# Kernel optimization log

Measured on AMD Instinct MI355X. Metric: run time of the kernel, lower is better.

Reference implementation:

```python
import jax, jax.numpy as jnp
import numpy as np


def _w1_1d(u, v):
    """POT-style 1D Wasserstein-1 between empirical dists of u and v (uniform weights).

    u, v: (N,) sample values. Follows ot.wasserstein_1d: sort samples, build
    cumulative weights, merge quantile levels, evaluate both quantile functions
    via searchsorted, and integrate |Q_u - Q_v| dq.
    """
    n = u.shape[0]
    u_s = jnp.sort(u)
    v_s = jnp.sort(v)
    # uniform weights -> identical cumulative weights for both distributions
    cw = jnp.cumsum(jnp.full((n,), 1.0 / n, dtype=u.dtype))
    qs = jnp.sort(jnp.concatenate([cw, cw]))  # (2N,) merged quantile levels
    idx = jnp.clip(jnp.searchsorted(cw, qs), 0, n - 1)  # quantile-function lookup
    uq = u_s[idx]
    vq = v_s[idx]
    delta = jnp.diff(qs, prepend=jnp.zeros((1,), dtype=u.dtype))  # dq segments
    return jnp.sum(delta * jnp.abs(uq - vq))


def setup_inputs() -> dict:
    key = jax.random.key(0)
    k1, k2 = jax.random.split(key)
    B, N = 4096, 4096
    return {
        "spectra_predict": jax.random.uniform(k1, (B, N), dtype=jnp.float32),
        "spectra_true": jax.random.uniform(k2, (B, N), dtype=jnp.float32),
    }


def reference(spectra_predict, spectra_true):
    # Original: wasserstein_1d(pred.T, true.T) batches over columns (= rows of
    # the untransposed [B, N] tensors), then mean over the batch.
    losses = jax.vmap(_w1_1d)(spectra_predict, spectra_true)  # (B,)
    return jnp.mean(losses)
```

## Files before the change

kernel.cpp:

```cpp
#include <hip/hip_runtime.h>


constexpr int N_ELEM  = 4096;
constexpr int V       = 32;
constexpr int THREADS = 256;

__device__ __forceinline__ float ce2(float x, float o, bool keep_min) {
    return ((o < x) != keep_min) ? x : o;
}

template<int S>
__device__ __forceinline__ void reg_merge(float r[V]) {
    #pragma unroll
    for (int k = 0; k < V; ++k) {
        if ((k & (S >> 1)) == 0) {
            const int j = k ^ (S - 1);
            const float a = r[k], b = r[j];
            r[k] = fminf(a, b);
            r[j] = fmaxf(a, b);
        }
    }
    #pragma unroll
    for (int s = S >> 2; s >= 1; s >>= 1) {
        #pragma unroll
        for (int k = 0; k < V; ++k) {
            if ((k & s) == 0) {
                const float a = r[k], b = r[k + s];
                r[k]     = fminf(a, b);
                r[k + s] = fmaxf(a, b);
            }
        }
    }
}

__device__ __forceinline__ void reg_tail_asc(float r[V]) {
    #pragma unroll
    for (int s = 16; s >= 1; s >>= 1) {
        #pragma unroll
        for (int k = 0; k < V; ++k) {
            if ((k & s) == 0) {
                const float a = r[k], b = r[k + s];
                r[k]     = fminf(a, b);
                r[k + s] = fmaxf(a, b);
            }
        }
    }
}

template<int CTRL>
__device__ __forceinline__ float dpp_x(float x) {
    return __int_as_float(__builtin_amdgcn_mov_dpp(__float_as_int(x), CTRL, 0xF, 0xF, true));
}
__device__ __forceinline__ float bperm_x(int pa, float x) {
    return __int_as_float(__builtin_amdgcn_ds_bpermute(pa, __float_as_int(x)));
}

template<int M>
__device__ __forceinline__ void xor_pass(float ru[V], float rv[V], int lane) {
    const bool keep_min = (lane & M) == 0;
    if constexpr (M == 1) {
        #pragma unroll
        for (int k = 0; k < V; ++k) {
            ru[k] = ce2(ru[k], dpp_x<0xB1>(ru[k]), keep_min);
            rv[k] = ce2(rv[k], dpp_x<0xB1>(rv[k]), keep_min);
        }
    } else if constexpr (M == 2) {
        #pragma unroll
        for (int k = 0; k < V; ++k) {
            ru[k] = ce2(ru[k], dpp_x<0x4E>(ru[k]), keep_min);
            rv[k] = ce2(rv[k], dpp_x<0x4E>(rv[k]), keep_min);
        }
    } else {
        const int pa = (lane ^ M) << 2;
        #pragma unroll
        for (int k = 0; k < V; ++k) {
            ru[k] = ce2(ru[k], bperm_x(pa, ru[k]), keep_min);
            rv[k] = ce2(rv[k], bperm_x(pa, rv[k]), keep_min);
        }
    }
}

template<int MMAX>
__device__ __forceinline__ void cross_descend(float ru[V], float rv[V], int lane) {
    if constexpr (MMAX >= 32) xor_pass<32>(ru, rv, lane);
    if constexpr (MMAX >= 16) xor_pass<16>(ru, rv, lane);
    if constexpr (MMAX >= 8)  xor_pass<8>(ru, rv, lane);
    if constexpr (MMAX >= 4)  xor_pass<4>(ru, rv, lane);
    if constexpr (MMAX >= 2)  xor_pass<2>(ru, rv, lane);
    if constexpr (MMAX >= 1)  xor_pass<1>(ru, rv, lane);
    reg_tail_asc(ru);
    reg_tail_asc(rv);
}

template<int X>
__device__ __forceinline__ void mirror_pass(float ru[V], float rv[V], int lane) {
    const bool keep_min = (lane & ((X + 1) >> 1)) == 0;
    if constexpr (X == 1) {
        #pragma unroll
        for (int k = 0; k < V / 2; ++k) {
            const int j = V - 1 - k;
            const float ua = dpp_x<0xB1>(ru[j]);
            const float ub = dpp_x<0xB1>(ru[k]);
            ru[k] = ce2(ru[k], ua, keep_min);
            ru[j] = ce2(ru[j], ub, keep_min);
            const float va = dpp_x<0xB1>(rv[j]);
            const float vb = dpp_x<0xB1>(rv[k]);
            rv[k] = ce2(rv[k], va, keep_min);
            rv[j] = ce2(rv[j], vb, keep_min);
        }
    } else {
        const int pa = (lane ^ X) << 2;
        #pragma unroll
        for (int k = 0; k < V / 2; ++k) {
            const int j = V - 1 - k;
            const float ua = bperm_x(pa, ru[j]);
            const float ub = bperm_x(pa, ru[k]);
            ru[k] = ce2(ru[k], ua, keep_min);
            ru[j] = ce2(ru[j], ub, keep_min);
            const float va = bperm_x(pa, rv[j]);
            const float vb = bperm_x(pa, rv[k]);
            rv[k] = ce2(rv[k], va, keep_min);
            rv[j] = ce2(rv[j], vb, keep_min);
        }
    }
}

template<int S>
__device__ __forceinline__ void stage_m(float ru[V], float rv[V], int lane) {
    mirror_pass<(S >> 5) - 1>(ru, rv, lane);
    cross_descend<(S >> 7)>(ru, rv, lane);
}

__global__ __launch_bounds__(THREADS, 5) void w1_rows_kernel(
    const float* __restrict__ pred,
    const float* __restrict__ tru,
    float* __restrict__ out,
    float scale)
{
    __shared__ float xbuf[128 * 33];
    __shared__ float wsum[THREADS / 64];

    const int tid  = threadIdx.x;
    const int t    = tid & 127;
    const int lane = tid & 63;
    const int row  = blockIdx.x * 2 + (tid >> 7);
    const size_t base = (size_t)row * N_ELEM + (size_t)t * V;

    float ru[V], rv[V];
    {
        const float4* u4 = (const float4*)(pred + base);
        const float4* v4 = (const float4*)(tru  + base);
        #pragma unroll
        for (int c = 0; c < V / 4; ++c) {
            float4 a = u4[c], b = v4[c];
            ru[4*c+0] = a.x; ru[4*c+1] = a.y; ru[4*c+2] = a.z; ru[4*c+3] = a.w;
            rv[4*c+0] = b.x; rv[4*c+1] = b.y; rv[4*c+2] = b.z; rv[4*c+3] = b.w;
        }
    }

    reg_merge<2>(ru);  reg_merge<2>(rv);
    reg_merge<4>(ru);  reg_merge<4>(rv);
    reg_merge<8>(ru);  reg_merge<8>(rv);
    reg_merge<16>(ru); reg_merge<16>(rv);
    reg_merge<32>(ru); reg_merge<32>(rv);

    stage_m<64>(ru, rv, lane);
    stage_m<128>(ru, rv, lane);
    stage_m<256>(ru, rv, lane);
    stage_m<512>(ru, rv, lane);
    stage_m<1024>(ru, rv, lane);
    stage_m<2048>(ru, rv, lane);

    {
        const bool is_upper = (t & 64) != 0;
        const int  slot_row = (tid >> 7) * 64;
        const int  my_base  = (slot_row + lane) * 33;
        const int  pa_base  = (slot_row + (63 - lane)) * 33;

        if (is_upper) {
            #pragma unroll
            for (int k = 0; k < V; ++k) xbuf[my_base + k] = ru[k];
        }
        __syncthreads();
        if (!is_upper) {
            #pragma unroll
            for (int k = 0; k < V; ++k) {
                const int  e = V - 1 - k;
                const float o  = xbuf[pa_base + e];
                const float mx = fmaxf(ru[k], o);
                ru[k] = fminf(ru[k], o);
                xbuf[pa_base + e] = mx;
            }
        }
        __syncthreads();
        if (is_upper) {
            #pragma unroll
            for (int k = 0; k < V; ++k) ru[k] = xbuf[my_base + k];
        }

        if (is_upper) {
            #pragma unroll
            for (int k = 0; k < V; ++k) xbuf[my_base + k] = rv[k];
        }
        __syncthreads();
        if (!is_upper) {
            #pragma unroll
            for (int k = 0; k < V; ++k) {
                const int  e = V - 1 - k;
                const float o  = xbuf[pa_base + e];
                const float mx = fmaxf(rv[k], o);
                rv[k] = fminf(rv[k], o);
                xbuf[pa_base + e] = mx;
            }
        }
        __syncthreads();
        if (is_upper) {
            #pragma unroll
            for (int k = 0; k < V; ++k) rv[k] = xbuf[my_base + k];
        }

        cross_descend<32>(ru, rv, lane);
    }

    float part = 0.f;
    #pragma unroll
    for (int k = 0; k < V; ++k) part += fabsf(ru[k] - rv[k]);

    #pragma unroll
    for (int off = 32; off > 0; off >>= 1)
        part += __shfl_down(part, off, 64);

    const int wid = tid >> 6;
    if (lane == 0) wsum[wid] = part;
    __syncthreads();
    if (tid == 0) {
        float tot = wsum[0] + wsum[1] + wsum[2] + wsum[3];
        atomicAdd(out, tot * scale);
    }
}

extern "C" void kernel_launch(void* const* d_in, const int* in_sizes, int n_in,
                              void* d_out, int out_size, void* d_ws, size_t ws_size,
                              hipStream_t stream)
{
    (void)n_in; (void)out_size; (void)d_ws; (void)ws_size;

    const float* pred = (const float*)d_in[0];
    const float* tru  = (const float*)d_in[1];
    float* out = (float*)d_out;

    const int B = in_sizes[0] / N_ELEM;

    hipMemsetAsync(out, 0, sizeof(float), stream);

    const float scale = 1.0f / ((float)N_ELEM * (float)B);
    w1_rows_kernel<<<B / 2, THREADS, 0, stream>>>(pred, tru, out, scale);
}
```

Measured before the change: 253.4 us.

## Replace compare-exchange with sign-flip fmin and DPP mirror/rotate networks

The cross-lane bitonic passes now flip the float sign bit in the upper lanes, so each compare-exchange becomes a single fminf with a negated partner in place of a compare plus select. The sign masks of consecutive passes are combined into one XOR per element. Several passes that used ds_bpermute (mirrors over 4, 8 and 16 lanes, and xor-8) now use DPP controls (quad reverse, row half-mirror, row mirror, row rotate), which cuts LDS permute traffic. Launch bounds drop from 5 to 4 waves to give the compiler more registers. The risks are the extra XOR instructions, lower occupancy, and the correctness of the DPP control encodings.

```diff
diff --git a/kernel.cpp b/kernel.cpp
--- a/kernel.cpp
+++ b/kernel.cpp
@@ -4,10 +4,6 @@
 constexpr int N_ELEM  = 4096;
 constexpr int V       = 32;
 constexpr int THREADS = 256;
-
-__device__ __forceinline__ float ce2(float x, float o, bool keep_min) {
-    return ((o < x) != keep_min) ? x : o;
-}
 
 template<int S>
 __device__ __forceinline__ void reg_merge(float r[V]) {
@@ -46,6 +42,10 @@
         }
     }
 }
+__device__ __forceinline__ void tail2(float ru[V], float rv[V]) {
+    reg_tail_asc(ru);
+    reg_tail_asc(rv);
+}
 
 template<int CTRL>
 __device__ __forceinline__ float dpp_x(float x) {
@@ -55,83 +55,68 @@
     return __int_as_float(__builtin_amdgcn_ds_bpermute(pa, __float_as_int(x)));
 }
 
-template<int M>
-__device__ __forceinline__ void xor_pass(float ru[V], float rv[V], int lane) {
-    const bool keep_min = (lane & M) == 0;
-    if constexpr (M == 1) {
-        #pragma unroll
-        for (int k = 0; k < V; ++k) {
-            ru[k] = ce2(ru[k], dpp_x<0xB1>(ru[k]), keep_min);
-            rv[k] = ce2(rv[k], dpp_x<0xB1>(rv[k]), keep_min);
-        }
-    } else if constexpr (M == 2) {
-        #pragma unroll
-        for (int k = 0; k < V; ++k) {
-            ru[k] = ce2(ru[k], dpp_x<0x4E>(ru[k]), keep_min);
-            rv[k] = ce2(rv[k], dpp_x<0x4E>(rv[k]), keep_min);
-        }
-    } else {
-        const int pa = (lane ^ M) << 2;
-        #pragma unroll
-        for (int k = 0; k < V; ++k) {
-            ru[k] = ce2(ru[k], bperm_x(pa, ru[k]), keep_min);
-            rv[k] = ce2(rv[k], bperm_x(pa, rv[k]), keep_min);
-        }
-    }
-}
-
-template<int MMAX>
-__device__ __forceinline__ void cross_descend(float ru[V], float rv[V], int lane) {
-    if constexpr (MMAX >= 32) xor_pass<32>(ru, rv, lane);
-    if constexpr (MMAX >= 16) xor_pass<16>(ru, rv, lane);
-    if constexpr (MMAX >= 8)  xor_pass<8>(ru, rv, lane);
-    if constexpr (MMAX >= 4)  xor_pass<4>(ru, rv, lane);
-    if constexpr (MMAX >= 2)  xor_pass<2>(ru, rv, lane);
-    if constexpr (MMAX >= 1)  xor_pass<1>(ru, rv, lane);
-    reg_tail_asc(ru);
-    reg_tail_asc(rv);
-}
-
-template<int X>
-__device__ __forceinline__ void mirror_pass(float ru[V], float rv[V], int lane) {
-    const bool keep_min = (lane & ((X + 1) >> 1)) == 0;
-    if constexpr (X == 1) {
-        #pragma unroll
-        for (int k = 0; k < V / 2; ++k) {
-            const int j = V - 1 - k;
-            const float ua = dpp_x<0xB1>(ru[j]);
-            const float ub = dpp_x<0xB1>(ru[k]);
-            ru[k] = ce2(ru[k], ua, keep_min);
-            ru[j] = ce2(ru[j], ub, keep_min);
-            const float va = dpp_x<0xB1>(rv[j]);
-            const float vb = dpp_x<0xB1>(rv[k]);
-            rv[k] = ce2(rv[k], va, keep_min);
-            rv[j] = ce2(rv[j], vb, keep_min);
-        }
-    } else {
-        const int pa = (lane ^ X) << 2;
-        #pragma unroll
-        for (int k = 0; k < V / 2; ++k) {
-            const int j = V - 1 - k;
-            const float ua = bperm_x(pa, ru[j]);
-            const float ub = bperm_x(pa, ru[k]);
-            ru[k] = ce2(ru[k], ua, keep_min);
-            ru[j] = ce2(ru[j], ub, keep_min);
-            const float va = bperm_x(pa, rv[j]);
-            const float vb = bperm_x(pa, rv[k]);
-            rv[k] = ce2(rv[k], va, keep_min);
-            rv[j] = ce2(rv[j], vb, keep_min);
-        }
-    }
-}
-
-template<int S>
-__device__ __forceinline__ void stage_m(float ru[V], float rv[V], int lane) {
-    mirror_pass<(S >> 5) - 1>(ru, rv, lane);
-    cross_descend<(S >> 7)>(ru, rv, lane);
-}
-
-__global__ __launch_bounds__(THREADS, 5) void w1_rows_kernel(
+__device__ __forceinline__ void trans(float r[V], unsigned m) {
+    #pragma unroll
+    for (int k = 0; k < V; ++k)
+        r[k] = __int_as_float(__float_as_int(r[k]) ^ m);
+}
+__device__ __forceinline__ void trans2(float ru[V], float rv[V], unsigned m) {
+    trans(ru, m);
+    trans(rv, m);
+}
+
+template<int CTRL>
+__device__ __forceinline__ void dppmin_pass(float ru[V], float rv[V]) {
+    #pragma unroll
+    for (int k = 0; k < V; ++k) {
+        ru[k] = fminf(ru[k], -dpp_x<CTRL>(ru[k]));
+        rv[k] = fminf(rv[k], -dpp_x<CTRL>(rv[k]));
+    }
+}
+__device__ __forceinline__ void bpermmin_pass(float ru[V], float rv[V], int pa) {
+    #pragma unroll
+    for (int k = 0; k < V; ++k) {
+        ru[k] = fminf(ru[k], -bperm_x(pa, ru[k]));
+        rv[k] = fminf(rv[k], -bperm_x(pa, rv[k]));
+    }
+}
+template<int CTRL>
+__device__ __forceinline__ void dppmin_mirror(float ru[V], float rv[V]) {
+    #pragma unroll
+    for (int k = 0; k < V / 2; ++k) {
+        const int j = V - 1 - k;
+        const float ua = dpp_x<CTRL>(ru[j]);
+        const float ub = dpp_x<CTRL>(ru[k]);
+        ru[k] = fminf(ru[k], -ua);
+        ru[j] = fminf(ru[j], -ub);
+        const float va = dpp_x<CTRL>(rv[j]);
+        const float vb = dpp_x<CTRL>(rv[k]);
+        rv[k] = fminf(rv[k], -va);
+        rv[j] = fminf(rv[j], -vb);
+    }
+}
+__device__ __forceinline__ void bpermmin_mirror(float ru[V], float rv[V], int pa) {
+    #pragma unroll
+    for (int k = 0; k < V / 2; ++k) {
+        const int j = V - 1 - k;
+        const float ua = bperm_x(pa, ru[j]);
+        const float ub = bperm_x(pa, ru[k]);
+        ru[k] = fminf(ru[k], -ua);
+        ru[j] = fminf(ru[j], -ub);
+        const float va = bperm_x(pa, rv[j]);
+        const float vb = bperm_x(pa, rv[k]);
+        rv[k] = fminf(rv[k], -va);
+        rv[j] = fminf(rv[j], -vb);
+    }
+}
+
+struct NegCtx {
+    unsigned s1, s2, s4, s8, s16, s32;
+    unsigned d21, d42, d84, d168, d3216;
+    int pa4, pa16, pa32, pm31, pm63;
+};
+
+__global__ __launch_bounds__(THREADS, 4) void w1_rows_kernel(
     const float* __restrict__ pred,
     const float* __restrict__ tru,
     float* __restrict__ out,
@@ -158,18 +143,89 @@
         }
     }
 
+    NegCtx M;
+    M.s1  = (lane & 1)  ? 0x80000000u : 0u;
+    M.s2  = (lane & 2)  ? 0x80000000u : 0u;
+    M.s4  = (lane & 4)  ? 0x80000000u : 0u;
+    M.s8  = (lane & 8)  ? 0x80000000u : 0u;
+    M.s16 = (lane & 16) ? 0x80000000u : 0u;
+    M.s32 = (lane & 32) ? 0x80000000u : 0u;
+    M.d21   = M.s2  ^ M.s1;
+    M.d42   = M.s4  ^ M.s2;
+    M.d84   = M.s8  ^ M.s4;
+    M.d168  = M.s16 ^ M.s8;
+    M.d3216 = M.s32 ^ M.s16;
+    M.pa4  = (lane ^ 4)  << 2;
+    M.pa16 = (lane ^ 16) << 2;
+    M.pa32 = (lane ^ 32) << 2;
+    M.pm31 = (lane ^ 31) << 2;
+    M.pm63 = (lane ^ 63) << 2;
+
     reg_merge<2>(ru);  reg_merge<2>(rv);
     reg_merge<4>(ru);  reg_merge<4>(rv);
     reg_merge<8>(ru);  reg_merge<8>(rv);
     reg_merge<16>(ru); reg_merge<16>(rv);
     reg_merge<32>(ru); reg_merge<32>(rv);
 
-    stage_m<64>(ru, rv, lane);
-    stage_m<128>(ru, rv, lane);
-    stage_m<256>(ru, rv, lane);
-    stage_m<512>(ru, rv, lane);
-    stage_m<1024>(ru, rv, lane);
-    stage_m<2048>(ru, rv, lane);
+    trans2(ru, rv, M.s1);
+    dppmin_mirror<0xB1>(ru, rv);
+    trans2(ru, rv, M.s1);
+    tail2(ru, rv);
+
+    trans2(ru, rv, M.s2);
+    dppmin_mirror<0x1B>(ru, rv);
+    trans2(ru, rv, M.d21);
+    dppmin_pass<0xB1>(ru, rv);
+    trans2(ru, rv, M.s1);
+    tail2(ru, rv);
+
+    trans2(ru, rv, M.s4);
+    dppmin_mirror<0x141>(ru, rv);
+    trans2(ru, rv, M.d42);
+    dppmin_pass<0x4E>(ru, rv);
+    trans2(ru, rv, M.d21);
+    dppmin_pass<0xB1>(ru, rv);
+    trans2(ru, rv, M.s1);
+    tail2(ru, rv);
+
+    trans2(ru, rv, M.s8);
+    dppmin_mirror<0x140>(ru, rv);
+    trans2(ru, rv, M.d84);
+    bpermmin_pass(ru, rv, M.pa4);
+    trans2(ru, rv, M.d42);
+    dppmin_pass<0x4E>(ru, rv);
+    trans2(ru, rv, M.d21);
+    dppmin_pass<0xB1>(ru, rv);
+    trans2(ru, rv, M.s1);
+    tail2(ru, rv);
+
+    trans2(ru, rv, M.s16);
+    bpermmin_mirror(ru, rv, M.pm31);
+    trans2(ru, rv, M.d168);
+    dppmin_pass<0x128>(ru, rv);
+    trans2(ru, rv, M.d84);
+    bpermmin_pass(ru, rv, M.pa4);
+    trans2(ru, rv, M.d42);
+    dppmin_pass<0x4E>(ru, rv);
+    trans2(ru, rv, M.d21);
+    dppmin_pass<0xB1>(ru, rv);
+    trans2(ru, rv, M.s1);
+    tail2(ru, rv);
+
+    trans2(ru, rv, M.s32);
+    bpermmin_mirror(ru, rv, M.pm63);
+    trans2(ru, rv, M.d3216);
+    bpermmin_pass(ru, rv, M.pa16);
+    trans2(ru, rv, M.d168);
+    dppmin_pass<0x128>(ru, rv);
+    trans2(ru, rv, M.d84);
+    bpermmin_pass(ru, rv, M.pa4);
+    trans2(ru, rv, M.d42);
+    dppmin_pass<0x4E>(ru, rv);
+    trans2(ru, rv, M.d21);
+    dppmin_pass<0xB1>(ru, rv);
+    trans2(ru, rv, M.s1);
+    tail2(ru, rv);
 
     {
         const bool is_upper = (t & 64) != 0;
@@ -219,7 +275,20 @@
             for (int k = 0; k < V; ++k) rv[k] = xbuf[my_base + k];
         }
 
-        cross_descend<32>(ru, rv, lane);
+        trans2(ru, rv, M.s32);
+        bpermmin_pass(ru, rv, M.pa32);
+        trans2(ru, rv, M.d3216);
+        bpermmin_pass(ru, rv, M.pa16);
+        trans2(ru, rv, M.d168);
+        dppmin_pass<0x128>(ru, rv);
+        trans2(ru, rv, M.d84);
+        bpermmin_pass(ru, rv, M.pa4);
+        trans2(ru, rv, M.d42);
+        dppmin_pass<0x4E>(ru, rv);
+        trans2(ru, rv, M.d21);
+        dppmin_pass<0xB1>(ru, rv);
+        trans2(ru, rv, M.s1);
+        tail2(ru, rv);
     }
 
     float part = 0.f;
```

Measured after the change: 279.1 us. +10.1%, slower.
